# Optimization experiments

Measured on AMD Instinct MI355X. Metric: run time of the kernel, lower is better.

Reference implementation:

```python
import jax, jax.numpy as jnp
import numpy as np

T, B, V, E, H, N = 256, 64, 50000, 256, 512, 6


def _lstm_dir(xg, m, W_hh, h0, c0, reverse):
    # xg: [T,B,4H] precomputed input projections; m: [T,B] float mask
    def step(carry, inp):
        h, c = carry
        xg_t, m_t = inp
        g = xg_t + h @ W_hh.T                      # [B,4H], PyTorch gate order i,f,g,o
        i, f, gg, o = jnp.split(g, 4, axis=-1)
        c_new = jax.nn.sigmoid(f) * c + jax.nn.sigmoid(i) * jnp.tanh(gg)
        h_new = jax.nn.sigmoid(o) * jnp.tanh(c_new)
        mm = m_t[:, None]
        h2 = mm * h_new + (1.0 - mm) * h
        c2 = mm * c_new + (1.0 - mm) * c
        return (h2, c2), h2 * mm                    # padded steps output 0 (pad_packed)
    _, hs = jax.lax.scan(step, (h0, c0), (xg, m), reverse=reverse)
    return hs                                       # [T,B,H]


def _crf_llh(emis, tags, mask, trans, start_trans, end_trans):
    # emis [T,B,N], tags [T,B], mask [T,B] int; torchcrf semantics, reduction='sum'
    mf = mask.astype(emis.dtype)
    Tn, Bn, Nn = emis.shape
    barange = jnp.arange(Bn)
    # numerator: score of gold path
    num = start_trans[tags[0]] + emis[0, barange, tags[0]]
    emit_sc = jnp.take_along_axis(emis, tags[..., None], axis=2)[..., 0]   # [T,B]
    trans_sc = trans[tags[:-1], tags[1:]]                                   # [T-1,B]
    num = num + jnp.sum((trans_sc + emit_sc[1:]) * mf[1:], axis=0)
    last_idx = jnp.sum(mask, axis=0).astype(jnp.int32) - 1                  # [B]
    num = num + end_trans[tags[last_idx, barange]]
    # denominator: forward algorithm (logsumexp scan over time)
    def step(score, inp):
        e_t, m_t = inp                                                      # [B,N],[B]
        nxt = jax.nn.logsumexp(score[:, :, None] + trans[None], axis=1) + e_t
        score = jnp.where(m_t[:, None] > 0, nxt, score)
        return score, None
    score0 = start_trans + emis[0]                                          # [B,N]
    score, _ = jax.lax.scan(step, score0, (emis[1:], mask[1:]))
    denom = jax.nn.logsumexp(score + end_trans, axis=1)                     # [B]
    return jnp.sum(num - denom)


def setup_inputs() -> dict:
    key = jax.random.key(0)
    ks = jax.random.split(key, 20)
    g = lambda k, sh, sc=0.05: (jax.random.normal(k, sh, jnp.float32) * sc)
    embed = g(ks[4], (V, E), 1.0).at[0].set(0.0)   # padding_idx=0
    return dict(
        sentence=jax.random.randint(ks[0], (T, B), 0, V),
        tags=jax.random.randint(ks[1], (T, B), 0, N),
        mask=jnp.ones((T, B), jnp.int32),
        h0=jax.random.normal(ks[2], (2, B, H), jnp.float32),
        c0=jax.random.normal(ks[3], (2, B, H), jnp.float32),
        embed=embed,
        W_ih_f=g(ks[5], (4 * H, E)), W_hh_f=g(ks[6], (4 * H, H)), b_f=g(ks[7], (4 * H,)),
        W_ih_b=g(ks[8], (4 * H, E)), W_hh_b=g(ks[9], (4 * H, H)), b_b=g(ks[10], (4 * H,)),
        W_out=g(ks[11], (N, 2 * H)), b_out=g(ks[12], (N,)),
        trans=g(ks[13], (N, N), 0.1), start_trans=g(ks[14], (N,), 0.1), end_trans=g(ks[15], (N,), 0.1),
    )


def reference(sentence, tags, mask, h0, c0, embed,
              W_ih_f, W_hh_f, b_f, W_ih_b, W_hh_b, b_b,
              W_out, b_out, trans, start_trans, end_trans):
    mf = mask.astype(jnp.float32)
    x = embed[sentence]                                         # [T,B,E]
    xg_f = jnp.einsum('tbe,ge->tbg', x, W_ih_f) + b_f           # [T,B,4H]
    xg_b = jnp.einsum('tbe,ge->tbg', x, W_ih_b) + b_b
    hf = _lstm_dir(xg_f, mf, W_hh_f, h0[0], c0[0], False)
    hb = _lstm_dir(xg_b, mf, W_hh_b, h0[1], c0[1], True)
    out = jnp.concatenate([hf, hb], axis=-1)                    # [T,B,2H]
    emis = jnp.einsum('tbh,nh->tbn', out, W_out) + b_out        # [T,B,N]
    return _crf_llh(emis, tags, mask, trans, start_trans, end_trans)
```

## Files before the change

kernel.cpp:

```cpp
#include <hip/hip_runtime.h>

typedef unsigned short ushort_t;
typedef unsigned int uint_t;
typedef __attribute__((ext_vector_type(8))) short short8;
typedef __attribute__((ext_vector_type(4))) float f32x4;
typedef __attribute__((ext_vector_type(4))) uint_t uint4a;
typedef __attribute__((ext_vector_type(2))) uint_t uint2a;

#define Tn 256
#define Bn 64
#define Hn 512
#define En 256
#define G4 2048
#define Nt 6

#define SENT 0x7FC07FC0u

__device__ inline ushort_t f2bf(float f) {
    uint_t u = __float_as_uint(f);
    uint_t r = u + 0x7FFFu + ((u >> 16) & 1u);
    return (ushort_t)(r >> 16);
}
__device__ inline float bf2f(ushort_t h) { return __uint_as_float(((uint_t)h) << 16); }
__device__ inline float sigm(float x) { return 1.f / (1.f + __expf(-x)); }
__device__ inline float tanh_(float x) { return 2.f / (1.f + __expf(-2.f * x)) - 1.f; }

__device__ inline uint4a gload16_sc1(const void* p) {
    uint4a r;
    asm volatile("global_load_dwordx4 %0, %1, off sc1" : "=v"(r) : "v"(p) : "memory");
    return r;
}
__device__ inline uint4a gload16_pl(const void* p) {
    uint4a r;
    asm volatile("global_load_dwordx4 %0, %1, off" : "=v"(r) : "v"(p) : "memory");
    return r;
}
__device__ inline int gload4_pl(const void* p) {
    int r;
    asm volatile("global_load_dword %0, %1, off" : "=v"(r) : "v"(p) : "memory");
    return r;
}
__device__ inline void gstore4_sc1(void* p, uint_t v) {
    asm volatile("global_store_dword %0, %1, off sc1" :: "v"(p), "v"(v) : "memory");
}
__device__ inline void vm_drain() { asm volatile("s_waitcnt vmcnt(0)" ::: "memory"); }

#define OFF_XBF    0u
#define OFF_WIH    8388608u
#define OFF_WHH    10485760u
#define OFF_HBUF   14680064u
#define OFF_EMIS   8388608u

#define SLOT_U     32768u
#define PANE_U     16384u
#define DIR_U      8421376u

__global__ void prep_kernel(const int* __restrict__ sent, const float* __restrict__ embed,
                            const float* __restrict__ Wihf, const float* __restrict__ Whhf,
                            const float* __restrict__ Wihb, const float* __restrict__ Whhb,
                            const float* __restrict__ h0, float* __restrict__ out,
                            ushort_t* __restrict__ x_bf, ushort_t* __restrict__ Wih_bf,
                            ushort_t* __restrict__ Whh_bf, ushort_t* __restrict__ hbuf) {
    long i = (long)blockIdx.x * 256 + threadIdx.x;
    const long nA = 524288, nB = 262144, nC = 1048576, nD = 32768, nE = 1048576;
    if (i < nA) {
        long e4 = i << 2;
        long d = e4 >> 20, r = e4 & 1048575;
        const float* W = d ? Whhb : Whhf;
        float4 v = *(const float4*)(W + r);
        uint2a pv;
        pv.x = (uint_t)f2bf(v.x) | ((uint_t)f2bf(v.y) << 16);
        pv.y = (uint_t)f2bf(v.z) | ((uint_t)f2bf(v.w) << 16);
        *(uint2a*)(Whh_bf + e4) = pv;
        return;
    }
    i -= nA;
    if (i < nB) {
        long e4 = i << 2;
        long d = e4 >> 19, r = e4 & 524287;
        const float* W = d ? Wihb : Wihf;
        float4 v = *(const float4*)(W + r);
        uint2a pv;
        pv.x = (uint_t)f2bf(v.x) | ((uint_t)f2bf(v.y) << 16);
        pv.y = (uint_t)f2bf(v.z) | ((uint_t)f2bf(v.w) << 16);
        *(uint2a*)(Wih_bf + (d << 19) + r) = pv;
        return;
    }
    i -= nB;
    if (i < nC) {
        long e4 = i << 2;
        long row = e4 >> 8, e = e4 & 255;
        int tok = sent[row];
        float4 v = *(const float4*)(embed + (size_t)tok * 256 + e);
        uint2a pv;
        pv.x = (uint_t)f2bf(v.x) | ((uint_t)f2bf(v.y) << 16);
        pv.y = (uint_t)f2bf(v.z) | ((uint_t)f2bf(v.w) << 16);
        *(uint2a*)(x_bf + e4) = pv;
        return;
    }
    i -= nC;
    if (i < nD) {
        long dir = i >> 14, rem = i & 16383;
        long b = rem >> 8, jw = rem & 255;
        const float* hp = h0 + (size_t)dir * Bn * Hn + (size_t)b * Hn + jw * 2;
        gstore4_sc1(hbuf + (size_t)dir * DIR_U + (b >> 5) * PANE_U
                         + (jw >> 3) * 512 + (b & 31) * 16 + 2 * (jw & 7),
                    (uint_t)f2bf(hp[0]) | ((uint_t)f2bf(hp[1]) << 16));
        return;
    }
    i -= nD;
    if (i < nE) {
        long dir = i >> 19, rem = i & 524287;
        ushort_t* p = hbuf + (size_t)dir * DIR_U + SLOT_U + (size_t)rem * 16;
        uint4a s; s.x = SENT; s.y = SENT; s.z = SENT; s.w = SENT;
        *(uint4a*)p = s;
        *(uint4a*)(p + 8) = s;
        return;
    }
    if (i == nE) { out[0] = 0.f; }
}

__global__ void __launch_bounds__(256, 1) lstm_kernel(
    const ushort_t* __restrict__ x_bf, const ushort_t* __restrict__ Wih_bf,
    const ushort_t* __restrict__ Whh_bf, const float* __restrict__ biasf,
    const float* __restrict__ biasb, const float* __restrict__ c0,
    const int* __restrict__ mask, ushort_t* __restrict__ hbuf) {

    __shared__ __align__(16) ushort_t x_s[2][32 * 264];
    __shared__ __align__(16) ushort_t h_s[32 * 520];
    __shared__ __align__(16) float gates_s[64 * 35];

    const int tid = threadIdx.x;
    const int wid = blockIdx.x;
    const int dir = wid >> 6;
    const int bh  = (wid >> 5) & 1;
    const int gs  = wid & 31;
    const int j0  = gs * 16;

    const int lane = tid & 63;
    const int wv = tid >> 6;
    const int qo = (lane >> 4) * 8;
    const int ml = lane & 15;

    const int grow = wv * 512 + j0 + ml;
    short8 bxf[8], bhf[16];
    {
        const ushort_t* wr = Wih_bf + (size_t)dir * G4 * En + (size_t)grow * En + qo;
        #pragma unroll
        for (int ks = 0; ks < 8; ++ks) bxf[ks] = *(const short8*)(wr + ks * 32);
        const ushort_t* wr2 = Whh_bf + (size_t)dir * G4 * Hn + (size_t)grow * Hn + qo;
        #pragma unroll
        for (int ks = 0; ks < 16; ++ks) bhf[ks] = *(const short8*)(wr2 + ks * 32);
    }
    const float bv = (dir ? biasb : biasf)[grow];

    const int jp = (tid & 7) * 2;
    const int bl = tid >> 3;
    const int bg = bh * 32 + bl;
    float creg[2];
    #pragma unroll
    for (int r = 0; r < 2; ++r)
        creg[r] = c0[(size_t)dir * Bn * Hn + (size_t)bg * Hn + j0 + jp + r];

    const ushort_t* xbase = x_bf + (size_t)bh * 32 * En;
    const ushort_t* hrd = hbuf + (size_t)dir * DIR_U + (size_t)bh * PANE_U;
    ushort_t*       hwr = hbuf + (size_t)dir * DIR_U + (size_t)bh * PANE_U;

    {
        const int t0 = dir ? (Tn - 1) : 0;
        const uint4* g4 = (const uint4*)(xbase + (size_t)t0 * Bn * En);
        uint4 xp[4];
        #pragma unroll
        for (int k = 0; k < 4; ++k) xp[k] = g4[tid + k * 256];
        #pragma unroll
        for (int k = 0; k < 4; ++k) {
            int c16 = tid + k * 256;
            *(uint4*)&x_s[0][(c16 >> 5) * 264 + (c16 & 31) * 8] = xp[k];
        }
    }
    int mv = mask[(dir ? (Tn - 1) : 0) * Bn + bg];
    __syncthreads();

    for (int s = 0; s < Tn; ++s) {
        const int cur = s & 1, nxt = cur ^ 1;

        const int sn = (s + 1 < Tn) ? s + 1 : Tn - 1;
        const int tn = dir ? (Tn - 1 - sn) : sn;
        uint4a xreg[4];
        {
            const ushort_t* g = xbase + (size_t)tn * Bn * En;
            #pragma unroll
            for (int k = 0; k < 4; ++k)
                xreg[k] = gload16_pl(g + (size_t)(tid + k * 256) * 8);
        }
        int mnx = gload4_pl(&mask[tn * Bn + bg]);
        const ushort_t* hp0 = hrd + (size_t)s * SLOT_U;
        uint4a hreg[8];
        #pragma unroll
        for (int k = 0; k < 8; ++k)
            hreg[k] = gload16_sc1(hp0 + (size_t)(tid + k * 256) * 8);

        f32x4 acc0, acc1;
        #pragma unroll
        for (int r = 0; r < 4; ++r) { acc0[r] = bv; acc1[r] = bv; }
        const ushort_t* xr0 = &x_s[cur][ml * 264 + qo];
        const ushort_t* xr1 = &x_s[cur][(16 + ml) * 264 + qo];
        #pragma unroll
        for (int ks = 0; ks < 8; ++ks) {
            short8 a0 = *(const short8*)(xr0 + ks * 32);
            short8 a1 = *(const short8*)(xr1 + ks * 32);
            acc0 = __builtin_amdgcn_mfma_f32_16x16x32_bf16(a0, bxf[ks], acc0, 0, 0, 0);
            acc1 = __builtin_amdgcn_mfma_f32_16x16x32_bf16(a1, bxf[ks], acc1, 0, 0, 0);
        }

        vm_drain();
        __builtin_amdgcn_sched_barrier(0);
        {
            uint_t okm = 0;
            #pragma unroll
            for (int k = 0; k < 8; ++k) {
                bool ok = true;
                #pragma unroll
                for (int w = 0; w < 4; ++w) ok &= (hreg[k][w] != SENT);
                okm |= (ok ? 1u : 0u) << k;
            }
            int guard = 65536;
            while (okm != 255u && --guard) {
                __builtin_amdgcn_s_sleep(1);
                #pragma unroll
                for (int k = 0; k < 8; ++k)
                    if (!((okm >> k) & 1))
                        hreg[k] = gload16_sc1(hp0 + (size_t)(tid + k * 256) * 8);
                vm_drain();
                __builtin_amdgcn_sched_barrier(0);
                #pragma unroll
                for (int k = 0; k < 8; ++k) {
                    if (!((okm >> k) & 1)) {
                        bool ok = true;
                        #pragma unroll
                        for (int w = 0; w < 4; ++w) ok &= (hreg[k][w] != SENT);
                        okm |= (ok ? 1u : 0u) << k;
                    }
                }
            }
        }
        #pragma unroll
        for (int k = 0; k < 8; ++k) {
            int c16 = tid + k * 256;
            int slice = c16 >> 6, w = c16 & 63;
            *(uint4a*)&h_s[(w >> 1) * 520 + slice * 16 + (w & 1) * 8] = hreg[k];
        }
        #pragma unroll
        for (int k = 0; k < 4; ++k) {
            int c16 = tid + k * 256;
            *(uint4a*)&x_s[nxt][(c16 >> 5) * 264 + (c16 & 31) * 8] = xreg[k];
        }
        __syncthreads();

        {
            const ushort_t* hr0 = &h_s[ml * 520 + qo];
            const ushort_t* hr1 = &h_s[(16 + ml) * 520 + qo];
            #pragma unroll
            for (int ks = 0; ks < 16; ++ks) {
                short8 a0 = *(const short8*)(hr0 + ks * 32);
                short8 a1 = *(const short8*)(hr1 + ks * 32);
                acc0 = __builtin_amdgcn_mfma_f32_16x16x32_bf16(a0, bhf[ks], acc0, 0, 0, 0);
                acc1 = __builtin_amdgcn_mfma_f32_16x16x32_bf16(a1, bhf[ks], acc1, 0, 0, 0);
            }
            int nl = wv * 16 + ml;
            int br = (lane >> 4) * 4;
            #pragma unroll
            for (int r = 0; r < 4; ++r) {
                gates_s[nl * 35 + br + r]      = acc0[r];
                gates_s[nl * 35 + 16 + br + r] = acc1[r];
            }
        }
        __syncthreads();

        {
            ushort_t hu[2];
            #pragma unroll
            for (int r = 0; r < 2; ++r) {
                int j = jp + r;
                float iv  = gates_s[j * 35 + bl];
                float fvv = gates_s[(16 + j) * 35 + bl];
                float gv  = gates_s[(32 + j) * 35 + bl];
                float ov  = gates_s[(48 + j) * 35 + bl];
                float cn = sigm(fvv) * creg[r] + sigm(iv) * tanh_(gv);
                float hn = sigm(ov) * tanh_(cn);
                float hp = bf2f(h_s[bl * 520 + j0 + j]);
                float h2;
                if (mv) { creg[r] = cn; h2 = hn; }
                else    { h2 = hp; }
                hu[r] = f2bf(h2);
            }
            gstore4_sc1(hwr + (size_t)(s + 1) * SLOT_U + (size_t)j0 * 32
                            + (size_t)bl * 16 + jp,
                        (uint_t)hu[0] | ((uint_t)hu[1] << 16));
        }
        mv = mnx;
        __syncthreads();
    }
}

__global__ void emis_kernel(const ushort_t* __restrict__ hbuf, const int* __restrict__ mask,
                            const float* __restrict__ Wout, const float* __restrict__ bout,
                            float* __restrict__ emis) {
    int row = blockIdx.x * 4 + (threadIdx.x >> 6);
    int lane = threadIdx.x & 63;
    int t = row >> 6, b = row & 63;
    float mf = mask[row] ? 1.f : 0.f;
    size_t slot = (lane < 32) ? (size_t)(t + 1) * SLOT_U
                              : (size_t)DIR_U + (size_t)(Tn - t) * SLOT_U;
    const ushort_t* hr = hbuf + slot + (size_t)(b >> 5) * PANE_U
                       + (size_t)(lane & 31) * 512 + (size_t)(b & 31) * 16;
    short8 h0v = *(const short8*)(hr);
    short8 h1v = *(const short8*)(hr + 8);
    float hv[16];
    #pragma unroll
    for (int j = 0; j < 8; ++j) {
        hv[j]     = bf2f((ushort_t)h0v[j]);
        hv[j + 8] = bf2f((ushort_t)h1v[j]);
    }
    float acc[6];
    #pragma unroll
    for (int n = 0; n < Nt; ++n) {
        const float* w = Wout + n * 1024 + lane * 16;
        float a = 0.f;
        #pragma unroll
        for (int j = 0; j < 16; ++j) a += hv[j] * w[j];
        acc[n] = a;
    }
    #pragma unroll
    for (int n = 0; n < Nt; ++n) {
        float v = acc[n];
        #pragma unroll
        for (int off = 32; off; off >>= 1) v += __shfl_down(v, off);
        if (lane == 0) emis[row * Nt + n] = v * mf + bout[n];
    }
}

__global__ void crf_kernel(const int* __restrict__ tags, const int* __restrict__ mask,
                           const float* __restrict__ emis, const float* __restrict__ trans,
                           const float* __restrict__ startt, const float* __restrict__ endt,
                           float* __restrict__ out) {
    int b = blockIdx.x;
    int lane = threadIdx.x;

    float part = 0.f;
    int mc = 0;
    for (int t = lane; t < Tn; t += 64) {
        int mv = mask[t * Bn + b];
        mc += mv;
        if (t >= 1) {
            int tp = tags[(t - 1) * Bn + b], tc = tags[t * Bn + b];
            part += (trans[tp * Nt + tc] + emis[(t * Bn + b) * Nt + tc]) * (float)mv;
        }
    }
    #pragma unroll
    for (int off = 32; off; off >>= 1) {
        part += __shfl_down(part, off);
        mc += __shfl_down(mc, off);
    }
    float num = 0.f;
    if (lane == 0) {
        int t0g = tags[b];
        num = startt[t0g] + emis[b * Nt + t0g] + part;
        int last = mc - 1;
        num += endt[tags[last * Bn + b]];
    }

    if (lane < Nt) {
        int j = lane;
        float tr[6];
        #pragma unroll
        for (int i = 0; i < Nt; ++i) tr[i] = trans[i * Nt + j];
        float score = startt[j] + emis[b * Nt + j];
        float e_nx = emis[(Bn + b) * Nt + j];
        int   m_nx = mask[Bn + b];
        for (int t = 1; t < Tn; ++t) {
            float e = e_nx;
            int mv = m_nx;
            if (t + 1 < Tn) {
                e_nx = emis[((t + 1) * Bn + b) * Nt + j];
                m_nx = mask[(t + 1) * Bn + b];
            }
            float v[6];
            float mx = -1e30f;
            #pragma unroll
            for (int i = 0; i < Nt; ++i) { v[i] = __shfl(score, i) + tr[i]; mx = fmaxf(mx, v[i]); }
            float sm = 0.f;
            #pragma unroll
            for (int i = 0; i < Nt; ++i) sm += __expf(v[i] - mx);
            float nxtv = mx + __logf(sm) + e;
            score = mv > 0 ? nxtv : score;
        }
        float fvv = score + endt[j];
        float m2 = fvv;
        #pragma unroll
        for (int i = 0; i < Nt; ++i) m2 = fmaxf(m2, __shfl(fvv, i));
        float s2 = 0.f;
        #pragma unroll
        for (int i = 0; i < Nt; ++i) s2 += __expf(__shfl(fvv, i) - m2);
        if (lane == 0) {
            float denom = m2 + __logf(s2);
            atomicAdd(out, num - denom);
        }
    }
}

extern "C" void kernel_launch(void* const* d_in, const int* in_sizes, int n_in,
                              void* d_out, int out_size, void* d_ws, size_t ws_size,
                              hipStream_t stream) {
    (void)in_sizes; (void)n_in; (void)out_size; (void)ws_size;
    const int*   sent  = (const int*)d_in[0];
    const int*   tags  = (const int*)d_in[1];
    const int*   mask  = (const int*)d_in[2];
    const float* h0    = (const float*)d_in[3];
    const float* c0    = (const float*)d_in[4];
    const float* embed = (const float*)d_in[5];
    const float* Wihf  = (const float*)d_in[6];
    const float* Whhf  = (const float*)d_in[7];
    const float* bf_   = (const float*)d_in[8];
    const float* Wihb  = (const float*)d_in[9];
    const float* Whhb  = (const float*)d_in[10];
    const float* bb_   = (const float*)d_in[11];
    const float* Wout  = (const float*)d_in[12];
    const float* bout  = (const float*)d_in[13];
    const float* trans = (const float*)d_in[14];
    const float* stt   = (const float*)d_in[15];
    const float* ent   = (const float*)d_in[16];
    float* out = (float*)d_out;
    char* ws = (char*)d_ws;

    ushort_t* x_bf   = (ushort_t*)(ws + OFF_XBF);
    ushort_t* Wih_bf = (ushort_t*)(ws + OFF_WIH);
    ushort_t* Whh_bf = (ushort_t*)(ws + OFF_WHH);
    ushort_t* hbuf   = (ushort_t*)(ws + OFF_HBUF);
    float*    emis   = (float*)(ws + OFF_EMIS);

    prep_kernel<<<11393, 256, 0, stream>>>(sent, embed, Wihf, Whhf, Wihb, Whhb,
                                           h0, out, x_bf, Wih_bf, Whh_bf, hbuf);
    lstm_kernel<<<128, 256, 0, stream>>>(x_bf, Wih_bf, Whh_bf, bf_, bb_, c0,
                                         mask, hbuf);
    emis_kernel<<<4096, 256, 0, stream>>>(hbuf, mask, Wout, bout, emis);
    crf_kernel<<<64, 64, 0, stream>>>(tags, mask, emis, trans, stt, ent, out);
}
```

Measured before the change: 988.3 us.

## Repartition LSTM workgroups into 16-batch quarters with 32 hidden units each

New measurement: 823.7 us. -16.7%, faster.

```diff
diff --git a/kernel.cpp b/kernel.cpp
--- a/kernel.cpp
+++ b/kernel.cpp
@@ -52,7 +52,7 @@
 #define OFF_EMIS   8388608u
 
 #define SLOT_U     32768u
-#define PANE_U     16384u
+#define BQ_U       8192u
 #define DIR_U      8421376u
 
 __global__ void prep_kernel(const int* __restrict__ sent, const float* __restrict__ embed,
@@ -102,9 +102,10 @@
     if (i < nD) {
         long dir = i >> 14, rem = i & 16383;
         long b = rem >> 8, jw = rem & 255;
-        const float* hp = h0 + (size_t)dir * Bn * Hn + (size_t)b * Hn + jw * 2;
-        gstore4_sc1(hbuf + (size_t)dir * DIR_U + (b >> 5) * PANE_U
-                         + (jw >> 3) * 512 + (b & 31) * 16 + 2 * (jw & 7),
+        long col = jw * 2;
+        const float* hp = h0 + (size_t)dir * Bn * Hn + (size_t)b * Hn + col;
+        gstore4_sc1(hbuf + (size_t)dir * DIR_U + (b >> 4) * BQ_U
+                         + (col >> 5) * 512 + (b & 15) * 32 + (col & 31),
                     (uint_t)f2bf(hp[0]) | ((uint_t)f2bf(hp[1]) << 16));
         return;
     }
@@ -126,54 +127,66 @@
     const float* __restrict__ biasb, const float* __restrict__ c0,
     const int* __restrict__ mask, ushort_t* __restrict__ hbuf) {
 
-    __shared__ __align__(16) ushort_t x_s[2][32 * 264];
-    __shared__ __align__(16) ushort_t h_s[32 * 520];
-    __shared__ __align__(16) float gates_s[64 * 35];
+    __shared__ __align__(16) ushort_t x_s[2][16 * 264];
+    __shared__ __align__(16) ushort_t h_s[16 * 520];
+    __shared__ __align__(16) float gates_s[128 * 17];
+    __shared__ ushort_t pad_s[20480];
 
     const int tid = threadIdx.x;
     const int wid = blockIdx.x;
     const int dir = wid >> 6;
-    const int bh  = (wid >> 5) & 1;
-    const int gs  = wid & 31;
-    const int j0  = gs * 16;
+    const int bq  = (wid >> 4) & 3;
+    const int sl  = wid & 15;
+    const int j0  = sl * 32;
+    if (tid == 0) pad_s[0] = 0;
 
     const int lane = tid & 63;
     const int wv = tid >> 6;
     const int qo = (lane >> 4) * 8;
     const int ml = lane & 15;
 
-    const int grow = wv * 512 + j0 + ml;
-    short8 bxf[8], bhf[16];
+    short8 bxf0[8], bxf1[8], bhf0[16], bhf1[16];
     {
-        const ushort_t* wr = Wih_bf + (size_t)dir * G4 * En + (size_t)grow * En + qo;
-        #pragma unroll
-        for (int ks = 0; ks < 8; ++ks) bxf[ks] = *(const short8*)(wr + ks * 32);
-        const ushort_t* wr2 = Whh_bf + (size_t)dir * G4 * Hn + (size_t)grow * Hn + qo;
-        #pragma unroll
-        for (int ks = 0; ks < 16; ++ks) bhf[ks] = *(const short8*)(wr2 + ks * 32);
-    }
-    const float bv = (dir ? biasb : biasf)[grow];
-
-    const int jp = (tid & 7) * 2;
-    const int bl = tid >> 3;
-    const int bg = bh * 32 + bl;
+        const int r0 = wv * 512 + j0 + ml;
+        const int r1 = r0 + 16;
+        const ushort_t* w0 = Wih_bf + (size_t)dir * G4 * En + (size_t)r0 * En + qo;
+        const ushort_t* w1 = Wih_bf + (size_t)dir * G4 * En + (size_t)r1 * En + qo;
+        #pragma unroll
+        for (int ks = 0; ks < 8; ++ks) {
+            bxf0[ks] = *(const short8*)(w0 + ks * 32);
+            bxf1[ks] = *(const short8*)(w1 + ks * 32);
+        }
+        const ushort_t* v0 = Whh_bf + (size_t)dir * G4 * Hn + (size_t)r0 * Hn + qo;
+        const ushort_t* v1 = Whh_bf + (size_t)dir * G4 * Hn + (size_t)r1 * Hn + qo;
+        #pragma unroll
+        for (int ks = 0; ks < 16; ++ks) {
+            bhf0[ks] = *(const short8*)(v0 + ks * 32);
+            bhf1[ks] = *(const short8*)(v1 + ks * 32);
+        }
+    }
+    const float* bias = dir ? biasb : biasf;
+    const float bv0 = bias[wv * 512 + j0 + ml];
+    const float bv1 = bias[wv * 512 + j0 + 16 + ml];
+
+    const int ub = tid >> 4;
+    const int uj = (tid & 15) * 2;
+    const int bg = bq * 16 + ub;
     float creg[2];
     #pragma unroll
     for (int r = 0; r < 2; ++r)
-        creg[r] = c0[(size_t)dir * Bn * Hn + (size_t)bg * Hn + j0 + jp + r];
-
-    const ushort_t* xbase = x_bf + (size_t)bh * 32 * En;
-    const ushort_t* hrd = hbuf + (size_t)dir * DIR_U + (size_t)bh * PANE_U;
-    ushort_t*       hwr = hbuf + (size_t)dir * DIR_U + (size_t)bh * PANE_U;
+        creg[r] = c0[(size_t)dir * Bn * Hn + (size_t)bg * Hn + j0 + uj + r];
+
+    const ushort_t* xbase = x_bf + (size_t)bq * 16 * En;
+    const size_t paneoff = (size_t)dir * DIR_U + (size_t)bq * BQ_U;
 
     {
         const int t0 = dir ? (Tn - 1) : 0;
         const uint4* g4 = (const uint4*)(xbase + (size_t)t0 * Bn * En);
-        uint4 xp[4];
-        #pragma unroll
-        for (int k = 0; k < 4; ++k) xp[k] = g4[tid + k * 256];
-        #pragma unroll
-        for (int k = 0; k < 4; ++k) {
+        uint4 xp[2];
+        #pragma unroll
+        for (int k = 0; k < 2; ++k) xp[k] = g4[tid + k * 256];
+        #pragma unroll
+        for (int k = 0; k < 2; ++k) {
             int c16 = tid + k * 256;
             *(uint4*)&x_s[0][(c16 >> 5) * 264 + (c16 & 31) * 8] = xp[k];
         }
@@ -186,31 +199,29 @@
 
         const int sn = (s + 1 < Tn) ? s + 1 : Tn - 1;
         const int tn = dir ? (Tn - 1 - sn) : sn;
-        uint4a xreg[4];
+        uint4a xreg[2];
         {
             const ushort_t* g = xbase + (size_t)tn * Bn * En;
             #pragma unroll
-            for (int k = 0; k < 4; ++k)
+            for (int k = 0; k < 2; ++k)
                 xreg[k] = gload16_pl(g + (size_t)(tid + k * 256) * 8);
         }
         int mnx = gload4_pl(&mask[tn * Bn + bg]);
-        const ushort_t* hp0 = hrd + (size_t)s * SLOT_U;
-        uint4a hreg[8];
-        #pragma unroll
-        for (int k = 0; k < 8; ++k)
+        const ushort_t* hp0 = hbuf + paneoff + (size_t)s * SLOT_U;
+        uint4a hreg[4];
+        #pragma unroll
+        for (int k = 0; k < 4; ++k)
             hreg[k] = gload16_sc1(hp0 + (size_t)(tid + k * 256) * 8);
 
         f32x4 acc0, acc1;
         #pragma unroll
-        for (int r = 0; r < 4; ++r) { acc0[r] = bv; acc1[r] = bv; }
+        for (int r = 0; r < 4; ++r) { acc0[r] = bv0; acc1[r] = bv1; }
         const ushort_t* xr0 = &x_s[cur][ml * 264 + qo];
-        const ushort_t* xr1 = &x_s[cur][(16 + ml) * 264 + qo];
         #pragma unroll
         for (int ks = 0; ks < 8; ++ks) {
-            short8 a0 = *(const short8*)(xr0 + ks * 32);
-            short8 a1 = *(const short8*)(xr1 + ks * 32);
-            acc0 = __builtin_amdgcn_mfma_f32_16x16x32_bf16(a0, bxf[ks], acc0, 0, 0, 0);
-            acc1 = __builtin_amdgcn_mfma_f32_16x16x32_bf16(a1, bxf[ks], acc1, 0, 0, 0);
+            short8 a = *(const short8*)(xr0 + ks * 32);
+            acc0 = __builtin_amdgcn_mfma_f32_16x16x32_bf16(a, bxf0[ks], acc0, 0, 0, 0);
+            acc1 = __builtin_amdgcn_mfma_f32_16x16x32_bf16(a, bxf1[ks], acc1, 0, 0, 0);
         }
 
         vm_drain();
@@ -218,23 +229,23 @@
         {
             uint_t okm = 0;
             #pragma unroll
-            for (int k = 0; k < 8; ++k) {
+            for (int k = 0; k < 4; ++k) {
                 bool ok = true;
                 #pragma unroll
                 for (int w = 0; w < 4; ++w) ok &= (hreg[k][w] != SENT);
                 okm |= (ok ? 1u : 0u) << k;
             }
             int guard = 65536;
-            while (okm != 255u && --guard) {
+            while (okm != 15u && --guard) {
                 __builtin_amdgcn_s_sleep(1);
                 #pragma unroll
-                for (int k = 0; k < 8; ++k)
+                for (int k = 0; k < 4; ++k)
                     if (!((okm >> k) & 1))
                         hreg[k] = gload16_sc1(hp0 + (size_t)(tid + k * 256) * 8);
                 vm_drain();
                 __builtin_amdgcn_sched_barrier(0);
                 #pragma unroll
-                for (int k = 0; k < 8; ++k) {
+                for (int k = 0; k < 4; ++k) {
                     if (!((okm >> k) & 1)) {
                         bool ok = true;
                         #pragma unroll
@@ -245,34 +256,32 @@
             }
         }
         #pragma unroll
-        for (int k = 0; k < 8; ++k) {
-            int c16 = tid + k * 256;
-            int slice = c16 >> 6, w = c16 & 63;
-            *(uint4a*)&h_s[(w >> 1) * 520 + slice * 16 + (w & 1) * 8] = hreg[k];
-        }
-        #pragma unroll
         for (int k = 0; k < 4; ++k) {
             int c16 = tid + k * 256;
+            int slc = c16 >> 6, b = (c16 >> 2) & 15, jc = c16 & 3;
+            *(uint4a*)&h_s[b * 520 + slc * 32 + jc * 8] = hreg[k];
+        }
+        #pragma unroll
+        for (int k = 0; k < 2; ++k) {
+            int c16 = tid + k * 256;
             *(uint4a*)&x_s[nxt][(c16 >> 5) * 264 + (c16 & 31) * 8] = xreg[k];
         }
         __syncthreads();
 
         {
             const ushort_t* hr0 = &h_s[ml * 520 + qo];
-            const ushort_t* hr1 = &h_s[(16 + ml) * 520 + qo];
             #pragma unroll
             for (int ks = 0; ks < 16; ++ks) {
-                short8 a0 = *(const short8*)(hr0 + ks * 32);
-                short8 a1 = *(const short8*)(hr1 + ks * 32);
-                acc0 = __builtin_amdgcn_mfma_f32_16x16x32_bf16(a0, bhf[ks], acc0, 0, 0, 0);
-                acc1 = __builtin_amdgcn_mfma_f32_16x16x32_bf16(a1, bhf[ks], acc1, 0, 0, 0);
-            }
-            int nl = wv * 16 + ml;
+                short8 a = *(const short8*)(hr0 + ks * 32);
+                acc0 = __builtin_amdgcn_mfma_f32_16x16x32_bf16(a, bhf0[ks], acc0, 0, 0, 0);
+                acc1 = __builtin_amdgcn_mfma_f32_16x16x32_bf16(a, bhf1[ks], acc1, 0, 0, 0);
+            }
+            int nl0 = wv * 32 + ml;
             int br = (lane >> 4) * 4;
             #pragma unroll
             for (int r = 0; r < 4; ++r) {
-                gates_s[nl * 35 + br + r]      = acc0[r];
-                gates_s[nl * 35 + 16 + br + r] = acc1[r];
+                gates_s[nl0 * 17 + br + r]        = acc0[r];
+                gates_s[(nl0 + 16) * 17 + br + r] = acc1[r];
             }
         }
         __syncthreads();
@@ -281,21 +290,21 @@
             ushort_t hu[2];
             #pragma unroll
             for (int r = 0; r < 2; ++r) {
-                int j = jp + r;
-                float iv  = gates_s[j * 35 + bl];
-                float fvv = gates_s[(16 + j) * 35 + bl];
-                float gv  = gates_s[(32 + j) * 35 + bl];
-                float ov  = gates_s[(48 + j) * 35 + bl];
+                int j = uj + r;
+                float iv  = gates_s[j * 17 + ub];
+                float fvv = gates_s[(32 + j) * 17 + ub];
+                float gv  = gates_s[(64 + j) * 17 + ub];
+                float ov  = gates_s[(96 + j) * 17 + ub];
                 float cn = sigm(fvv) * creg[r] + sigm(iv) * tanh_(gv);
                 float hn = sigm(ov) * tanh_(cn);
-                float hp = bf2f(h_s[bl * 520 + j0 + j]);
+                float hp = bf2f(h_s[ub * 520 + j0 + j]);
                 float h2;
                 if (mv) { creg[r] = cn; h2 = hn; }
                 else    { h2 = hp; }
                 hu[r] = f2bf(h2);
             }
-            gstore4_sc1(hwr + (size_t)(s + 1) * SLOT_U + (size_t)j0 * 32
-                            + (size_t)bl * 16 + jp,
+            gstore4_sc1(hbuf + paneoff + (size_t)(s + 1) * SLOT_U
+                             + (size_t)sl * 512 + (size_t)ub * 32 + uj,
                         (uint_t)hu[0] | ((uint_t)hu[1] << 16));
         }
         mv = mnx;
@@ -312,8 +321,10 @@
     float mf = mask[row] ? 1.f : 0.f;
     size_t slot = (lane < 32) ? (size_t)(t + 1) * SLOT_U
                               : (size_t)DIR_U + (size_t)(Tn - t) * SLOT_U;
-    const ushort_t* hr = hbuf + slot + (size_t)(b >> 5) * PANE_U
-                       + (size_t)(lane & 31) * 512 + (size_t)(b & 31) * 16;
+    int l5 = lane & 31;
+    const ushort_t* hr = hbuf + slot + (size_t)(b >> 4) * BQ_U
+                       + (size_t)(l5 >> 1) * 512 + (size_t)(b & 15) * 32
+                       + (size_t)(l5 & 1) * 16;
     short8 h0v = *(const short8*)(hr);
     short8 h1v = *(const short8*)(hr + 8);
     float hv[16];
```
